# Performance work log

Measured on AMD Instinct MI355X. Metric: run time of the kernel, lower is better.

## Reference

```python
import jax, jax.numpy as jnp
import numpy as np

B, S, D, H = 2, 2048, 1024, 16
DK = D // H  # 64
EPS = 1e-10
ROPE_BASE = 500000.0


def _rms_norm(x, w):
    # RMSNorm over last dim: w * x / sqrt(mean(x^2) + eps)
    return w * x * jax.lax.rsqrt(jnp.mean(x * x, axis=-1, keepdims=True) + EPS)


def _rope_tables(seq_len, dk):
    inv_freq = 1.0 / (ROPE_BASE ** (jnp.arange(0, dk, 2, dtype=jnp.float32) / dk))
    t = jnp.arange(seq_len, dtype=jnp.float32)
    freqs = jnp.outer(t, inv_freq)            # (S, dk/2)
    emb = jnp.concatenate([freqs, freqs], -1)  # (S, dk)
    return jnp.cos(emb), jnp.sin(emb)


def _rotate_half(x):
    x1, x2 = jnp.split(x, 2, axis=-1)
    return jnp.concatenate([-x2, x1], axis=-1)


def setup_inputs() -> dict:
    key = jax.random.key(0)
    ks = jax.random.split(key, 8)
    scale = 1.0 / np.sqrt(D)
    return {
        "q": jax.random.normal(ks[0], (B, S, D), jnp.float32),
        "k": jax.random.normal(ks[1], (B, S, D), jnp.float32),
        "v": jax.random.normal(ks[2], (B, S, D), jnp.float32),
        "Wq": jax.random.normal(ks[3], (D, D), jnp.float32) * scale,
        "Wk": jax.random.normal(ks[4], (D, D), jnp.float32) * scale,
        "Wv": jax.random.normal(ks[5], (D, D), jnp.float32) * scale,
        "Wo": jax.random.normal(ks[6], (D, D), jnp.float32) * scale,
        "q_norm_w": jnp.ones((DK,), jnp.float32) + 0.02 * jax.random.normal(ks[7], (DK,), jnp.float32),
        "k_norm_w": jnp.ones((DK,), jnp.float32),
    }


def reference(q, k, v, Wq, Wk, Wv, Wo, q_norm_w, k_norm_w):
    Bq, Sq, _ = q.shape
    # Projections (torch Linear: x @ W.T), split into heads -> (B, H, S, DK)
    def proj(x, W):
        return (x @ W.T).reshape(Bq, Sq, H, DK).transpose(0, 2, 1, 3)
    query, key_, value = proj(q, Wq), proj(k, Wk), proj(v, Wv)
    # Per-head QK RMSNorm
    query = _rms_norm(query, q_norm_w)
    key_ = _rms_norm(key_, k_norm_w)
    # RoPE
    cos, sin = _rope_tables(Sq, DK)  # (S, DK) each; broadcast over (B, H)
    query = query * cos + _rotate_half(query) * sin
    key_ = key_ * cos + _rotate_half(key_) * sin
    # Causal attention
    scale = 1.0 / np.sqrt(DK)
    scores = jnp.einsum("bhqd,bhkd->bhqk", query, key_) * scale
    causal = jnp.tril(jnp.ones((Sq, Sq), bool))
    scores = jnp.where(causal, scores, -jnp.inf)
    probs = jax.nn.softmax(scores, axis=-1)
    attn = jnp.einsum("bhqk,bhkd->bhqd", probs, value)
    # Merge heads and output projection
    attn = attn.transpose(0, 2, 1, 3).reshape(Bq, Sq, D)
    return attn @ Wo.T
```

## Files before the change

kernel.cpp:

```cpp
#include <hip/hip_runtime.h>
#include <hip/hip_bf16.h>
#include <math.h>

#define B_  2
#define S_  2048
#define D_  1024
#define H_  16
#define DK_ 64

typedef __attribute__((ext_vector_type(8))) short bf16x8;
typedef __attribute__((ext_vector_type(4))) float f32x4;

#define MFMA_BF16(a, b, c) __builtin_amdgcn_mfma_f32_16x16x32_bf16((a), (b), (c), 0, 0, 0)

#define QSCALE 0.18033688011112042f
#define ROPE_L2 0.591611512f

__device__ __forceinline__ unsigned short f2bf(float f) {
  unsigned int u = __float_as_uint(f);
  u += 0x7FFFu + ((u >> 16) & 1u);
  return (unsigned short)(u >> 16);
}

__device__ __forceinline__ void gl_lds16(const void* g, void* l) {
  __builtin_amdgcn_global_load_lds(
      (const __attribute__((address_space(1))) void*)g,
      (__attribute__((address_space(3))) void*)l, 16, 0, 0);
}

__device__ __forceinline__ int lsw(int row, int col) {
  return row * 64 + ((((col) >> 3) ^ (row & 7)) << 3) + (col & 7);
}

__global__ __launch_bounds__(256)
void cvt_bf16(const float* __restrict__ q, const float* __restrict__ k,
              const float* __restrict__ v, const float* __restrict__ wq,
              const float* __restrict__ wk, const float* __restrict__ wv,
              const float* __restrict__ wo,
              unsigned short* __restrict__ qb, unsigned short* __restrict__ kb,
              unsigned short* __restrict__ vb, unsigned short* __restrict__ wqb,
              unsigned short* __restrict__ wkb, unsigned short* __restrict__ wvb,
              unsigned short* __restrict__ wob) {
  const float* src; unsigned short* dst; int n;
  switch (blockIdx.y) {
    case 0: src = q;  dst = qb;  n = B_ * S_ * D_; break;
    case 1: src = k;  dst = kb;  n = B_ * S_ * D_; break;
    case 2: src = v;  dst = vb;  n = B_ * S_ * D_; break;
    case 3: src = wq; dst = wqb; n = D_ * D_; break;
    case 4: src = wk; dst = wkb; n = D_ * D_; break;
    case 5: src = wv; dst = wvb; n = D_ * D_; break;
    default: src = wo; dst = wob; n = D_ * D_; break;
  }
  for (int i = (blockIdx.x * 256 + threadIdx.x) * 4; i < n; i += 768 * 256 * 4) {
    float4 val = *(const float4*)&src[i];
    ushort4 r4;
    r4.x = f2bf(val.x); r4.y = f2bf(val.y); r4.z = f2bf(val.z); r4.w = f2bf(val.w);
    *(ushort4*)&dst[i] = r4;
  }
}

__global__ __launch_bounds__(256)
void gemm_qkv(const unsigned short* __restrict__ qa, const unsigned short* __restrict__ ka,
              const unsigned short* __restrict__ va,
              const unsigned short* __restrict__ wq, const unsigned short* __restrict__ wk,
              const unsigned short* __restrict__ wv,
              unsigned short* __restrict__ Qo, unsigned short* __restrict__ Ko,
              unsigned short* __restrict__ Vto,
              const float* __restrict__ qnw, const float* __restrict__ knw) {
  __shared__ unsigned short As[2][128 * 32];
  __shared__ unsigned short Bs[2][128 * 32];
  const int bid = blockIdx.x;
  const int r8 = bid & 7;
  const int bxj = (bid >> 3) & 7;
  const int g = bid >> 6;
  const int zy = r8 * 12 + g;
  const int z = zy >> 5, by = zy & 31;
  const unsigned short* A = (z == 0) ? qa : (z == 1) ? ka : va;
  const unsigned short* W = (z == 0) ? wq : (z == 1) ? wk : wv;

  const int t = threadIdx.x, lane = t & 63, wave = t >> 6;
  const int l16 = lane & 15, quad = lane >> 4;
  const int wm = wave >> 1, wn = wave & 1;
  const int m0 = by * 128, j0 = bxj * 128;

  f32x4 acc[4][4];
#pragma unroll
  for (int i = 0; i < 4; ++i)
#pragma unroll
    for (int j = 0; j < 4; ++j) acc[i][j] = (f32x4)(0.0f);

  auto stage = [&](int kb, int buf) {
#pragma unroll
    for (int i = 0; i < 2; ++i) {
      const int c  = (wave * 2 + i) * 64 + lane;
      const int r  = c >> 2;
      const int co = (c & 3) * 8;
      gl_lds16(&A[(size_t)(m0 + r) * D_ + kb + co], &As[buf][(wave * 2 + i) * 512]);
      gl_lds16(&W[(size_t)(j0 + r) * D_ + kb + co], &Bs[buf][(wave * 2 + i) * 512]);
    }
  };

  stage(0, 0);
  for (int kb = 0; kb < D_; kb += 32) {
    const int buf = (kb >> 5) & 1;
    __syncthreads();
    if (kb + 32 < D_) stage(kb + 32, buf ^ 1);

    bf16x8 af[4], bfr[4];
#pragma unroll
    for (int mi = 0; mi < 4; ++mi)
      af[mi] = *(const bf16x8*)&As[buf][(wm * 64 + mi * 16 + l16) * 32 + quad * 8];
#pragma unroll
    for (int ni = 0; ni < 4; ++ni)
      bfr[ni] = *(const bf16x8*)&Bs[buf][(wn * 64 + ni * 16 + l16) * 32 + quad * 8];
#pragma unroll
    for (int mi = 0; mi < 4; ++mi)
#pragma unroll
      for (int ni = 0; ni < 4; ++ni)
        acc[mi][ni] = MFMA_BF16(af[mi], bfr[ni], acc[mi][ni]);
  }

  const int h = bxj * 2 + wn;
  if (z == 2) {
#pragma unroll
    for (int mi = 0; mi < 4; ++mi) {
      const int rowb = m0 + wm * 64 + mi * 16 + quad * 4;
      const int b = rowb >> 11, s0 = rowb & (S_ - 1);
#pragma unroll
      for (int ni = 0; ni < 4; ++ni) {
        const int dk = ni * 16 + l16;
        const unsigned int u0 =
            (unsigned int)f2bf(acc[mi][ni][0]) | ((unsigned int)f2bf(acc[mi][ni][1]) << 16);
        const unsigned int u1 =
            (unsigned int)f2bf(acc[mi][ni][2]) | ((unsigned int)f2bf(acc[mi][ni][3]) << 16);
        *(uint2*)&Vto[((size_t)((b * H_ + h) * DK_ + dk)) * S_ + s0] = make_uint2(u0, u1);
      }
    }
  } else {
    unsigned short* out = (z == 0) ? Qo : Ko;
    const float* nw = (z == 0) ? qnw : knw;
    const float sc  = (z == 0) ? QSCALE : 1.0f;
    float wv_[4];
#pragma unroll
    for (int ni = 0; ni < 4; ++ni) wv_[ni] = nw[ni * 16 + l16];
    const float invA = exp2f(-(float)l16 * ROPE_L2);
    const float invB = exp2f(-(float)(16 + l16) * ROPE_L2);
#pragma unroll
    for (int mi = 0; mi < 4; ++mi) {
#pragma unroll
      for (int r = 0; r < 4; ++r) {
        const int rowg = m0 + wm * 64 + mi * 16 + quad * 4 + r;
        const int b = rowg >> 11, s = rowg & (S_ - 1);
        float ss = 0.f;
#pragma unroll
        for (int ni = 0; ni < 4; ++ni) ss += acc[mi][ni][r] * acc[mi][ni][r];
#pragma unroll
        for (int m = 1; m < 16; m <<= 1) ss += __shfl_xor(ss, m);
        const float rms = rsqrtf(ss * (1.0f / DK_) + 1e-10f);
        float xn[4];
#pragma unroll
        for (int ni = 0; ni < 4; ++ni) xn[ni] = wv_[ni] * acc[mi][ni][r] * rms;
        const float fA = (float)s * invA, fB = (float)s * invB;
        const float cA = __cosf(fA) * sc, sA = __sinf(fA) * sc;
        const float cB = __cosf(fB) * sc, sB = __sinf(fB) * sc;
        float o0 = xn[0] * cA - xn[2] * sA;
        float o1 = xn[1] * cB - xn[3] * sB;
        float o2 = xn[2] * cA + xn[0] * sA;
        float o3 = xn[3] * cB + xn[1] * sB;
        const size_t base = ((size_t)(b * H_ + h) * S_ + s) * DK_;
        out[base +  0 + l16] = f2bf(o0);
        out[base + 16 + l16] = f2bf(o1);
        out[base + 32 + l16] = f2bf(o2);
        out[base + 48 + l16] = f2bf(o3);
      }
    }
  }
}

__global__ __launch_bounds__(256)
void flash3(const unsigned short* __restrict__ Q, const unsigned short* __restrict__ K,
            const unsigned short* __restrict__ Vt, unsigned short* __restrict__ Oa) {
  __shared__ unsigned short Ks[2][64 * 64];
  __shared__ unsigned short Vs[2][64 * 64];
  __shared__ unsigned short Ps[64 * 64];
  const int bx = blockIdx.x;
  const int idx = bx >> 5;
  const int qt = (idx < 16) ? idx : (47 - idx);
  const int bh = bx & 31;
  const int t = threadIdx.x, lane = t & 63, wave = t >> 6;
  const int l16 = lane & 15, quad = lane >> 4;
  const size_t hb = (size_t)bh * S_ * DK_;
  const unsigned short* Qh  = Q + hb;
  const unsigned short* Kh  = K + hb;
  const unsigned short* Vth = Vt + hb;

  bf16x8 qf[2];
#pragma unroll
  for (int ks = 0; ks < 2; ++ks)
    qf[ks] = *(const bf16x8*)
      &Qh[(size_t)(qt * 64 + wave * 16 + l16) * DK_ + ks * 32 + quad * 8];

  bf16x8 ones;
#pragma unroll
  for (int j = 0; j < 8; ++j) ones[j] = (short)0x3F80;

  f32x4 o[4], lacc;
  lacc = (f32x4)(0.0f);
#pragma unroll
  for (int ni = 0; ni < 4; ++ni) o[ni] = (f32x4)(0.0f);

  auto stage = [&](int kt, int bufi) {
#pragma unroll
    for (int i = 0; i < 2; ++i) {
      const int rbase = wave * 16 + i * 8;
      const int r = rbase + (lane >> 3);
      const int c = ((lane & 7) ^ (r & 7)) * 8;
      gl_lds16(&Kh[(size_t)(kt * 64 + r) * DK_ + c], &Ks[bufi][rbase * 64]);
      gl_lds16(&Vth[(size_t)r * S_ + kt * 64 + c], &Vs[bufi][rbase * 64]);
    }
  };

  const int nkt = qt + 1;
  stage(0, 0);
  for (int kt = 0; kt < nkt; ++kt) {
    const int buf = kt & 1;
    __syncthreads();
    if (kt + 1 < nkt) stage(kt + 1, buf ^ 1);

    f32x4 sv[4];
#pragma unroll
    for (int kvi = 0; kvi < 4; ++kvi) sv[kvi] = (f32x4)(0.0f);
#pragma unroll
    for (int ks = 0; ks < 2; ++ks) {
      bf16x8 ak[4];
#pragma unroll
      for (int kvi = 0; kvi < 4; ++kvi)
        ak[kvi] = *(const bf16x8*)&Ks[buf][lsw(kvi * 16 + l16, ks * 32 + quad * 8)];
#pragma unroll
      for (int kvi = 0; kvi < 4; ++kvi)
        sv[kvi] = MFMA_BF16(ak[kvi], qf[ks], sv[kvi]);
    }

    float p[4][4];
    if (kt == qt) {
      const int qg = qt * 64 + wave * 16 + l16;
#pragma unroll
      for (int kvi = 0; kvi < 4; ++kvi)
#pragma unroll
        for (int r = 0; r < 4; ++r) {
          float x = sv[kvi][r];
          if ((kt * 64 + kvi * 16 + quad * 4 + r) > qg) x = -INFINITY;
          p[kvi][r] = exp2f(x);
        }
    } else {
#pragma unroll
      for (int kvi = 0; kvi < 4; ++kvi)
#pragma unroll
        for (int r = 0; r < 4; ++r) p[kvi][r] = exp2f(sv[kvi][r]);
    }

#pragma unroll
    for (int kvi = 0; kvi < 4; ++kvi) {
      const unsigned int d0 =
          (__float_as_uint(p[kvi][1]) & 0xFFFF0000u) | (__float_as_uint(p[kvi][0]) >> 16);
      const unsigned int d1 =
          (__float_as_uint(p[kvi][3]) & 0xFFFF0000u) | (__float_as_uint(p[kvi][2]) >> 16);
      *(uint2*)&Ps[lsw(wave * 16 + l16, kvi * 16 + quad * 4)] = make_uint2(d0, d1);
    }
    asm volatile("s_waitcnt lgkmcnt(0)" ::: "memory");

#pragma unroll
    for (int ks = 0; ks < 2; ++ks) {
      bf16x8 ap, bv[4];
      ap = *(const bf16x8*)&Ps[lsw(wave * 16 + l16, ks * 32 + quad * 8)];
#pragma unroll
      for (int ni = 0; ni < 4; ++ni)
        bv[ni] = *(const bf16x8*)&Vs[buf][lsw(ni * 16 + l16, ks * 32 + quad * 8)];
#pragma unroll
      for (int ni = 0; ni < 4; ++ni)
        o[ni] = MFMA_BF16(ap, bv[ni], o[ni]);
      lacc = MFMA_BF16(ap, ones, lacc);
    }
  }

  const int b = bh >> 4, h = bh & 15;
#pragma unroll
  for (int r = 0; r < 4; ++r) {
    const int srow = qt * 64 + wave * 16 + quad * 4 + r;
    const float linv = 1.0f / lacc[r];
#pragma unroll
    for (int ni = 0; ni < 4; ++ni)
      Oa[((size_t)(b * S_ + srow) * H_ + h) * DK_ + ni * 16 + l16] =
          f2bf(o[ni][r] * linv);
  }
}

__global__ __launch_bounds__(256)
void gemm_out(const unsigned short* __restrict__ A, const unsigned short* __restrict__ W,
              float* __restrict__ out) {
  __shared__ unsigned short As[2][128 * 32];
  __shared__ unsigned short Bs[2][64 * 32];
  const int bid = blockIdx.x;
  const int r8 = bid & 7;
  const int g = (bid >> 3) & 3;
  const int by = r8 * 4 + g;
  const int bxj = bid >> 5;
  const int t = threadIdx.x, lane = t & 63, wave = t >> 6;
  const int l16 = lane & 15, quad = lane >> 4;
  const int wm = wave >> 1, wn = wave & 1;
  const int m0 = by * 128, j0 = bxj * 64;

  f32x4 acc[4][2];
#pragma unroll
  for (int i = 0; i < 4; ++i)
#pragma unroll
    for (int j = 0; j < 2; ++j) acc[i][j] = (f32x4)(0.0f);

  auto stage = [&](int kb, int buf) {
#pragma unroll
    for (int i = 0; i < 2; ++i) {
      const int c  = (wave * 2 + i) * 64 + lane;
      const int r  = c >> 2;
      const int co = (c & 3) * 8;
      gl_lds16(&A[(size_t)(m0 + r) * D_ + kb + co], &As[buf][(wave * 2 + i) * 512]);
    }
    {
      const int c  = wave * 64 + lane;
      const int r  = c >> 2;
      const int co = (c & 3) * 8;
      gl_lds16(&W[(size_t)(j0 + r) * D_ + kb + co], &Bs[buf][wave * 512]);
    }
  };

  stage(0, 0);
  for (int kb = 0; kb < D_; kb += 32) {
    const int buf = (kb >> 5) & 1;
    __syncthreads();
    if (kb + 32 < D_) stage(kb + 32, buf ^ 1);

    bf16x8 af[4], bfr[2];
#pragma unroll
    for (int mi = 0; mi < 4; ++mi)
      af[mi] = *(const bf16x8*)&As[buf][(wm * 64 + mi * 16 + l16) * 32 + quad * 8];
#pragma unroll
    for (int ni = 0; ni < 2; ++ni)
      bfr[ni] = *(const bf16x8*)&Bs[buf][(wn * 32 + ni * 16 + l16) * 32 + quad * 8];
#pragma unroll
    for (int mi = 0; mi < 4; ++mi)
#pragma unroll
      for (int ni = 0; ni < 2; ++ni)
        acc[mi][ni] = MFMA_BF16(af[mi], bfr[ni], acc[mi][ni]);
  }

#pragma unroll
  for (int mi = 0; mi < 4; ++mi) {
    const int rowb = m0 + wm * 64 + mi * 16 + quad * 4;
#pragma unroll
    for (int ni = 0; ni < 2; ++ni) {
      const int col = j0 + wn * 32 + ni * 16 + l16;
#pragma unroll
      for (int r = 0; r < 4; ++r)
        out[(size_t)(rowb + r) * D_ + col] = acc[mi][ni][r];
    }
  }
}

extern "C" void kernel_launch(void* const* d_in, const int* in_sizes, int n_in,
                              void* d_out, int out_size, void* d_ws, size_t ws_size,
                              hipStream_t stream) {
  (void)in_sizes; (void)n_in; (void)out_size; (void)ws_size;
  const float* q  = (const float*)d_in[0];
  const float* k  = (const float*)d_in[1];
  const float* v  = (const float*)d_in[2];
  const float* Wq = (const float*)d_in[3];
  const float* Wk = (const float*)d_in[4];
  const float* Wv = (const float*)d_in[5];
  const float* Wo = (const float*)d_in[6];
  const float* qw = (const float*)d_in[7];
  const float* kw = (const float*)d_in[8];

  char* ws = (char*)d_ws;
  const size_t MB = 1u << 20;
  unsigned short* qb  = (unsigned short*)(ws + 0 * MB);
  unsigned short* kb  = (unsigned short*)(ws + 8 * MB);
  unsigned short* vb  = (unsigned short*)(ws + 16 * MB);
  unsigned short* wqb = (unsigned short*)(ws + 24 * MB);
  unsigned short* wkb = (unsigned short*)(ws + 26 * MB);
  unsigned short* wvb = (unsigned short*)(ws + 28 * MB);
  unsigned short* wob = (unsigned short*)(ws + 30 * MB);
  unsigned short* Qb  = (unsigned short*)(ws + 32 * MB);
  unsigned short* Kb  = (unsigned short*)(ws + 40 * MB);
  unsigned short* Vtb = (unsigned short*)(ws + 48 * MB);
  unsigned short* Ab  = (unsigned short*)(ws + 56 * MB);

  cvt_bf16<<<dim3(768, 7), 256, 0, stream>>>(q, k, v, Wq, Wk, Wv, Wo,
                                             qb, kb, vb, wqb, wkb, wvb, wob);

  gemm_qkv<<<768, 256, 0, stream>>>(qb, kb, vb, wqb, wkb, wvb, Qb, Kb, Vtb, qw, kw);

  flash3<<<1024, 256, 0, stream>>>(Qb, Kb, Vtb, Ab);

  gemm_out<<<512, 256, 0, stream>>>(Ab, wob, (float*)d_out);
}
```

Baseline: 218.5 us.

## Double query tile per flash block to reuse K/V tiles across 128 rows

The attention kernel now handles 128 query rows per block instead of 64, with each wave owning two 16-row MFMA sub-tiles. Each K/V tile staged into LDS is therefore reused for twice as many query rows, which halves K/V global and LDS traffic per output and halves the grid to 512 blocks. In exchange, each thread holds more registers (doubled accumulators and scores), there are fewer blocks for load balancing, and the diagonal tile now masks across two KV tiles, adding some wasted work on masked entries.

```diff
diff --git a/kernel.cpp b/kernel.cpp
--- a/kernel.cpp
+++ b/kernel.cpp
@@ -178,14 +178,14 @@
 }
 
 __global__ __launch_bounds__(256)
-void flash3(const unsigned short* __restrict__ Q, const unsigned short* __restrict__ K,
+void flash6(const unsigned short* __restrict__ Q, const unsigned short* __restrict__ K,
             const unsigned short* __restrict__ Vt, unsigned short* __restrict__ Oa) {
   __shared__ unsigned short Ks[2][64 * 64];
   __shared__ unsigned short Vs[2][64 * 64];
-  __shared__ unsigned short Ps[64 * 64];
+  __shared__ unsigned short Ps[128 * 64];
   const int bx = blockIdx.x;
   const int idx = bx >> 5;
-  const int qt = (idx < 16) ? idx : (47 - idx);
+  const int qt = (idx < 8) ? idx : (23 - idx);
   const int bh = bx & 31;
   const int t = threadIdx.x, lane = t & 63, wave = t >> 6;
   const int l16 = lane & 15, quad = lane >> 4;
@@ -193,21 +193,27 @@
   const unsigned short* Qh  = Q + hb;
   const unsigned short* Kh  = K + hb;
   const unsigned short* Vth = Vt + hb;
-
-  bf16x8 qf[2];
-#pragma unroll
-  for (int ks = 0; ks < 2; ++ks)
-    qf[ks] = *(const bf16x8*)
-      &Qh[(size_t)(qt * 64 + wave * 16 + l16) * DK_ + ks * 32 + quad * 8];
+  const int m0 = qt * 128;
+
+  bf16x8 qf[2][2];
+#pragma unroll
+  for (int mi = 0; mi < 2; ++mi)
+#pragma unroll
+    for (int ks = 0; ks < 2; ++ks)
+      qf[mi][ks] = *(const bf16x8*)
+        &Qh[(size_t)(m0 + wave * 32 + mi * 16 + l16) * DK_ + ks * 32 + quad * 8];
 
   bf16x8 ones;
 #pragma unroll
   for (int j = 0; j < 8; ++j) ones[j] = (short)0x3F80;
 
-  f32x4 o[4], lacc;
-  lacc = (f32x4)(0.0f);
-#pragma unroll
-  for (int ni = 0; ni < 4; ++ni) o[ni] = (f32x4)(0.0f);
+  f32x4 o[2][4], lacc[2];
+#pragma unroll
+  for (int mi = 0; mi < 2; ++mi) {
+    lacc[mi] = (f32x4)(0.0f);
+#pragma unroll
+    for (int ni = 0; ni < 4; ++ni) o[mi][ni] = (f32x4)(0.0f);
+  }
 
   auto stage = [&](int kt, int bufi) {
 #pragma unroll
@@ -220,16 +226,18 @@
     }
   };
 
-  const int nkt = qt + 1;
+  const int nkt = 2 * qt + 2;
   stage(0, 0);
   for (int kt = 0; kt < nkt; ++kt) {
     const int buf = kt & 1;
     __syncthreads();
     if (kt + 1 < nkt) stage(kt + 1, buf ^ 1);
 
-    f32x4 sv[4];
-#pragma unroll
-    for (int kvi = 0; kvi < 4; ++kvi) sv[kvi] = (f32x4)(0.0f);
+    f32x4 sv[4][2];
+#pragma unroll
+    for (int kvi = 0; kvi < 4; ++kvi)
+#pragma unroll
+      for (int mi = 0; mi < 2; ++mi) sv[kvi][mi] = (f32x4)(0.0f);
 #pragma unroll
     for (int ks = 0; ks < 2; ++ks) {
       bf16x8 ak[4];
@@ -238,61 +246,79 @@
         ak[kvi] = *(const bf16x8*)&Ks[buf][lsw(kvi * 16 + l16, ks * 32 + quad * 8)];
 #pragma unroll
       for (int kvi = 0; kvi < 4; ++kvi)
-        sv[kvi] = MFMA_BF16(ak[kvi], qf[ks], sv[kvi]);
-    }
-
-    float p[4][4];
-    if (kt == qt) {
-      const int qg = qt * 64 + wave * 16 + l16;
+#pragma unroll
+        for (int mi = 0; mi < 2; ++mi)
+          sv[kvi][mi] = MFMA_BF16(ak[kvi], qf[mi][ks], sv[kvi][mi]);
+    }
+
+    float p[4][2][4];
+    if (kt >= 2 * qt) {
 #pragma unroll
       for (int kvi = 0; kvi < 4; ++kvi)
 #pragma unroll
-        for (int r = 0; r < 4; ++r) {
-          float x = sv[kvi][r];
-          if ((kt * 64 + kvi * 16 + quad * 4 + r) > qg) x = -INFINITY;
-          p[kvi][r] = exp2f(x);
+        for (int mi = 0; mi < 2; ++mi) {
+          const int qg = m0 + wave * 32 + mi * 16 + l16;
+          const int kvb = kt * 64 + kvi * 16 + quad * 4;
+#pragma unroll
+          for (int r = 0; r < 4; ++r) {
+            float x = sv[kvi][mi][r];
+            if ((kvb + r) > qg) x = -INFINITY;
+            p[kvi][mi][r] = exp2f(x);
+          }
         }
     } else {
 #pragma unroll
       for (int kvi = 0; kvi < 4; ++kvi)
 #pragma unroll
-        for (int r = 0; r < 4; ++r) p[kvi][r] = exp2f(sv[kvi][r]);
-    }
-
-#pragma unroll
-    for (int kvi = 0; kvi < 4; ++kvi) {
-      const unsigned int d0 =
-          (__float_as_uint(p[kvi][1]) & 0xFFFF0000u) | (__float_as_uint(p[kvi][0]) >> 16);
-      const unsigned int d1 =
-          (__float_as_uint(p[kvi][3]) & 0xFFFF0000u) | (__float_as_uint(p[kvi][2]) >> 16);
-      *(uint2*)&Ps[lsw(wave * 16 + l16, kvi * 16 + quad * 4)] = make_uint2(d0, d1);
-    }
+        for (int mi = 0; mi < 2; ++mi)
+#pragma unroll
+          for (int r = 0; r < 4; ++r) p[kvi][mi][r] = exp2f(sv[kvi][mi][r]);
+    }
+
+#pragma unroll
+    for (int kvi = 0; kvi < 4; ++kvi)
+#pragma unroll
+      for (int mi = 0; mi < 2; ++mi) {
+        const unsigned int d0 = (__float_as_uint(p[kvi][mi][1]) & 0xFFFF0000u) |
+                                (__float_as_uint(p[kvi][mi][0]) >> 16);
+        const unsigned int d1 = (__float_as_uint(p[kvi][mi][3]) & 0xFFFF0000u) |
+                                (__float_as_uint(p[kvi][mi][2]) >> 16);
+        *(uint2*)&Ps[lsw(wave * 32 + mi * 16 + l16, kvi * 16 + quad * 4)] =
+            make_uint2(d0, d1);
+      }
     asm volatile("s_waitcnt lgkmcnt(0)" ::: "memory");
 
 #pragma unroll
     for (int ks = 0; ks < 2; ++ks) {
-      bf16x8 ap, bv[4];
-      ap = *(const bf16x8*)&Ps[lsw(wave * 16 + l16, ks * 32 + quad * 8)];
+      bf16x8 ap[2], bv[4];
+#pragma unroll
+      for (int mi = 0; mi < 2; ++mi)
+        ap[mi] = *(const bf16x8*)&Ps[lsw(wave * 32 + mi * 16 + l16, ks * 32 + quad * 8)];
 #pragma unroll
       for (int ni = 0; ni < 4; ++ni)
         bv[ni] = *(const bf16x8*)&Vs[buf][lsw(ni * 16 + l16, ks * 32 + quad * 8)];
 #pragma unroll
+      for (int mi = 0; mi < 2; ++mi) {
+#pragma unroll
+        for (int ni = 0; ni < 4; ++ni)
+          o[mi][ni] = MFMA_BF16(ap[mi], bv[ni], o[mi][ni]);
+        lacc[mi] = MFMA_BF16(ap[mi], ones, lacc[mi]);
+      }
+    }
+  }
+
+  const int b = bh >> 4, h = bh & 15;
+#pragma unroll
+  for (int mi = 0; mi < 2; ++mi)
+#pragma unroll
+    for (int r = 0; r < 4; ++r) {
+      const int srow = m0 + wave * 32 + mi * 16 + quad * 4 + r;
+      const float linv = 1.0f / lacc[mi][r];
+#pragma unroll
       for (int ni = 0; ni < 4; ++ni)
-        o[ni] = MFMA_BF16(ap, bv[ni], o[ni]);
-      lacc = MFMA_BF16(ap, ones, lacc);
-    }
-  }
-
-  const int b = bh >> 4, h = bh & 15;
-#pragma unroll
-  for (int r = 0; r < 4; ++r) {
-    const int srow = qt * 64 + wave * 16 + quad * 4 + r;
-    const float linv = 1.0f / lacc[r];
-#pragma unroll
-    for (int ni = 0; ni < 4; ++ni)
-      Oa[((size_t)(b * S_ + srow) * H_ + h) * DK_ + ni * 16 + l16] =
-          f2bf(o[ni][r] * linv);
-  }
+        Oa[((size_t)(b * S_ + srow) * H_ + h) * DK_ + ni * 16 + l16] =
+            f2bf(o[mi][ni][r] * linv);
+    }
 }
 
 __global__ __launch_bounds__(256)
@@ -398,7 +424,7 @@
 
   gemm_qkv<<<768, 256, 0, stream>>>(qb, kb, vb, wqb, wkb, wvb, Qb, Kb, Vtb, qw, kw);
 
-  flash3<<<1024, 256, 0, stream>>>(Qb, Kb, Vtb, Ab);
+  flash6<<<512, 256, 0, stream>>>(Qb, Kb, Vtb, Ab);
 
   gemm_out<<<512, 256, 0, stream>>>(Ab, wob, (float*)d_out);
 }
```

Measured after the change: 231.5 us. 6.0% more time.
